# Kernel optimization log

Measured on AMD Instinct MI355X. Metric: run time of the kernel, lower is better.

## Reference

```python
import jax, jax.numpy as jnp
import numpy as np
from jax import lax

B, T, K = 2048, 1024, 8  # batch, max seq len, num_tags


def setup_inputs() -> dict:
    key = jax.random.key(0)
    k1, k2, k3, k4, k5, k6, k7 = jax.random.split(key, 7)
    score = jax.random.normal(k1, (B, T, K), jnp.float32)
    log_p = jax.nn.log_softmax(jax.random.normal(k2, (B, T, K), jnp.float32), axis=-1)
    tags = jax.random.randint(k3, (B, T), 0, K)
    seq_l = jax.random.randint(k4, (B,), 1, T + 1)  # valid lengths in [1, T]
    transitions = jax.random.normal(k5, (K, K), jnp.float32) * 0.1
    start_transitions = jax.random.normal(k6, (K,), jnp.float32) * 0.1
    end_transitions = jax.random.normal(k7, (K,), jnp.float32) * 0.1
    return {
        "log_p": log_p,
        "score": score,
        "transitions": transitions,
        "start_transitions": start_transitions,
        "end_transitions": end_transitions,
        "tags": tags,
        "seq_l": seq_l,
    }


def _crf_nll(score, tags, mask, transitions, start_transitions, end_transitions):
    """Linear-chain CRF negative log-likelihood, summed over the batch.
    score: [B,T,K] emissions; tags: [B,T] gold; mask: [B,T] bool."""
    maskf = mask.astype(score.dtype)

    # ---- numerator: score of the gold tag path ----
    emit = jnp.take_along_axis(score, tags[..., None], axis=-1)[..., 0]  # [B,T]
    num = (emit * maskf).sum(-1)
    num = num + start_transitions[tags[:, 0]]
    trans_sc = transitions[tags[:, :-1], tags[:, 1:]]  # [B,T-1]
    num = num + (trans_sc * maskf[:, 1:]).sum(-1)
    last_idx = (mask.sum(-1).astype(jnp.int32) - 1)  # [B]
    last_tag = jnp.take_along_axis(tags, last_idx[:, None], axis=1)[:, 0]
    num = num + end_transitions[last_tag]

    # ---- denominator: log partition via log-sum-exp scan over time ----
    alpha0 = start_transitions[None, :] + score[:, 0]  # [B,K]

    def step(alpha, xs):
        emit_t, mask_t = xs  # [B,K], [B]
        # alpha[b,i] + transitions[i,j] + emit[b,j], logsumexp over i
        nxt = jax.nn.logsumexp(alpha[:, :, None] + transitions[None, :, :], axis=1) + emit_t
        alpha = jnp.where(mask_t[:, None], nxt, alpha)  # freeze past end-of-seq
        return alpha, None

    xs = (jnp.swapaxes(score[:, 1:], 0, 1), jnp.swapaxes(mask[:, 1:], 0, 1))
    alpha, _ = lax.scan(step, alpha0, xs)
    log_z = jax.nn.logsumexp(alpha + end_transitions[None, :], axis=-1)  # [B]

    return -(num - log_z).sum()


def reference(log_p, score, transitions, start_transitions, end_transitions, tags, seq_l):
    mask = jnp.arange(T)[None, :] < seq_l[:, None]  # [B,T] bool
    loss = _crf_nll(score, tags, mask, transitions, start_transitions, end_transitions) / B
    # training path: quick predictions = argmax over per-token log_p, zero-padded
    pred_idx = jnp.argmax(log_p, axis=-1) * mask.astype(jnp.int64)
    return loss, pred_idx
```

## Files before the change

### kernel.cpp

```cpp
#include <hip/hip_runtime.h>
#include <hip/hip_bf16.h>


namespace {

constexpr int B = 2048;
constexpr int T = 1024;
constexpr int K = 8;
constexpr int CL = 64;
constexpr int NC = T / CL;

__device__ __forceinline__ float max8(const float* a) {
  return fmaxf(fmaxf(fmaxf(a[0], a[1]), fmaxf(a[2], a[3])),
               fmaxf(fmaxf(a[4], a[5]), fmaxf(a[6], a[7])));
}

__global__ __launch_bounds__(256) void pred_num_kernel(
    const float* __restrict__ log_p, const float* __restrict__ score,
    const float* __restrict__ trans, const float* __restrict__ start_tr,
    const float* __restrict__ end_tr, const int* __restrict__ tags,
    const int* __restrict__ seq_l, float* __restrict__ out_pred,
    float* __restrict__ ws_num) {
  int g = blockIdx.x * blockDim.x + threadIdx.x;
  int b = g >> 10;
  int t = g & (T - 1);

  const float4* lp = reinterpret_cast<const float4*>(log_p) + (g << 1);
  float4 u0 = lp[0], u1 = lp[1];
  float v[8] = {u0.x, u0.y, u0.z, u0.w, u1.x, u1.y, u1.z, u1.w};
  int best = 0;
  float bv = v[0];
#pragma unroll
  for (int j = 1; j < 8; ++j) {
    if (v[j] > bv) { bv = v[j]; best = j; }
  }

  int L = seq_l[b];
  bool act = (t < L);
  out_pred[g] = act ? (float)best : 0.0f;

  float contrib = 0.0f;
  if (act) {
    int tg = tags[g];
    contrib = score[g * 8 + tg];
    if (t == 0)
      contrib += start_tr[tg];
    else
      contrib += trans[tags[g - 1] * 8 + tg];
    if (t == L - 1) contrib += end_tr[tg];
  }
#pragma unroll
  for (int off = 32; off >= 1; off >>= 1) contrib += __shfl_down(contrib, off);
  if ((threadIdx.x & 63) == 0) atomicAdd(&ws_num[b], contrib);
}

__global__ __launch_bounds__(256) void chunk_kernel(
    const float* __restrict__ score, const float* __restrict__ trans,
    const int* __restrict__ seq_l, float* __restrict__ wsA,
    float* __restrict__ wsS) {
  int g = blockIdx.x * blockDim.x + threadIdx.x;
  int k = g & 7;
  int c = (g >> 3) & (NC - 1);
  int b = g >> 7;

  float E[8][8];
#pragma unroll
  for (int i = 0; i < 8; ++i)
#pragma unroll
    for (int j = 0; j < 8; ++j) E[i][j] = __expf(trans[i * 8 + j]);

  float a[8];
#pragma unroll
  for (int j = 0; j < 8; ++j) a[j] = (j == k) ? 1.0f : 0.0f;
  float sig = 0.0f;

  int L = seq_l[b];
  int t0 = c * CL;
  int ts = (c == 0) ? 1 : t0;
  int te = min(t0 + CL, L);
  int n = te - ts;
  const float* sp = score + ((size_t)b * T + ts) * 8;

  for (int it = 0; it < n; ++it) {
    float4 sA = *reinterpret_cast<const float4*>(sp);
    float4 sB = *reinterpret_cast<const float4*>(sp + 4);
    sp += 8;
    float em[8] = {__expf(sA.x), __expf(sA.y), __expf(sA.z), __expf(sA.w),
                   __expf(sB.x), __expf(sB.y), __expf(sB.z), __expf(sB.w)};
    float na[8];
#pragma unroll
    for (int j = 0; j < 8; ++j) {
      float acc = E[0][j] * a[0];
#pragma unroll
      for (int i = 1; i < 8; ++i) acc = fmaf(E[i][j], a[i], acc);
      na[j] = em[j] * acc;
    }
#pragma unroll
    for (int j = 0; j < 8; ++j) a[j] = na[j];
    if ((it & 7) == 7) {
      float mm = max8(a);
      float r = __builtin_amdgcn_rcpf(mm);
#pragma unroll
      for (int j = 0; j < 8; ++j) a[j] *= r;
      sig += __logf(mm);
    }
  }
  {
    float mm = max8(a);
    if (mm > 0.0f) {
      float r = __builtin_amdgcn_rcpf(mm);
#pragma unroll
      for (int j = 0; j < 8; ++j) a[j] *= r;
      sig += __logf(mm);
    }
  }

  float* Ao = wsA + (size_t)(((b * NC + c) * 8 + k) * 8);
  *reinterpret_cast<float4*>(Ao) = make_float4(a[0], a[1], a[2], a[3]);
  *reinterpret_cast<float4*>(Ao + 4) = make_float4(a[4], a[5], a[6], a[7]);
  wsS[(b * NC + c) * 8 + k] = sig;
}

__global__ __launch_bounds__(256) void combine_kernel(
    const float* __restrict__ score, const float* __restrict__ start_tr,
    const float* __restrict__ end_tr, const float* __restrict__ wsA,
    const float* __restrict__ wsS, const float* __restrict__ ws_num,
    float* __restrict__ out_loss) {
  int b = blockIdx.x * blockDim.x + threadIdx.x;

  const float* s0 = score + (size_t)b * T * 8;
  float p[8];
#pragma unroll
  for (int j = 0; j < 8; ++j) p[j] = __expf(start_tr[j] + s0[j]);
  float tau = 0.0f;
  {
    float mm = max8(p);
    float r = __builtin_amdgcn_rcpf(mm);
#pragma unroll
    for (int j = 0; j < 8; ++j) p[j] *= r;
    tau += __logf(mm);
  }

  float een[8];
#pragma unroll
  for (int j = 0; j < 8; ++j) een[j] = __expf(end_tr[j]);

  for (int c = 0; c < NC; ++c) {
    const float* Ab = wsA + (size_t)((b * NC + c) * 64);
    const float* Sb = wsS + (b * NC + c) * 8;
    float sg[8];
#pragma unroll
    for (int j = 0; j < 8; ++j) sg[j] = Sb[j];
    float smax = max8(sg);
    float w[8];
#pragma unroll
    for (int j = 0; j < 8; ++j) w[j] = p[j] * __expf(sg[j] - smax);

    float Am[8][8];
#pragma unroll
    for (int i = 0; i < 8; ++i) {
      float4 q0 = *reinterpret_cast<const float4*>(Ab + i * 8);
      float4 q1 = *reinterpret_cast<const float4*>(Ab + i * 8 + 4);
      Am[i][0] = q0.x; Am[i][1] = q0.y; Am[i][2] = q0.z; Am[i][3] = q0.w;
      Am[i][4] = q1.x; Am[i][5] = q1.y; Am[i][6] = q1.z; Am[i][7] = q1.w;
    }
    float np[8];
#pragma unroll
    for (int j = 0; j < 8; ++j) {
      float acc = Am[0][j] * w[0];
#pragma unroll
      for (int i = 1; i < 8; ++i) acc = fmaf(Am[i][j], w[i], acc);
      np[j] = acc;
    }
    tau += smax;
    float mm = max8(np);
    float r = __builtin_amdgcn_rcpf(mm);
#pragma unroll
    for (int j = 0; j < 8; ++j) p[j] = np[j] * r;
    tau += __logf(mm);
  }

  float acc = 0.0f;
#pragma unroll
  for (int j = 0; j < 8; ++j) acc = fmaf(p[j], een[j], acc);
  float logz = tau + __logf(acc);

  float part = (logz - ws_num[b]) * (1.0f / (float)B);
#pragma unroll
  for (int off = 32; off >= 1; off >>= 1) part += __shfl_down(part, off);
  if ((threadIdx.x & 63) == 0) atomicAdd(out_loss, part);
}

}

extern "C" void kernel_launch(void* const* d_in, const int* in_sizes, int n_in,
                              void* d_out, int out_size, void* d_ws,
                              size_t ws_size, hipStream_t stream) {
  const float* log_p = (const float*)d_in[0];
  const float* score = (const float*)d_in[1];
  const float* trans = (const float*)d_in[2];
  const float* start_tr = (const float*)d_in[3];
  const float* end_tr = (const float*)d_in[4];
  const int* tags = (const int*)d_in[5];
  const int* seq_l = (const int*)d_in[6];
  float* out = (float*)d_out;

  float* wsA = (float*)d_ws;
  float* wsS = wsA + (size_t)B * NC * 64;
  float* wsNum = wsS + (size_t)B * NC * 8;

  hipMemsetAsync(wsNum, 0, B * sizeof(float), stream);
  hipMemsetAsync(out, 0, sizeof(float), stream);

  pred_num_kernel<<<(B * T) / 256, 256, 0, stream>>>(
      log_p, score, trans, start_tr, end_tr, tags, seq_l, out + 1, wsNum);
  chunk_kernel<<<(B * NC * 8) / 256, 256, 0, stream>>>(score, trans, seq_l,
                                                       wsA, wsS);
  combine_kernel<<<B / 256, 256, 0, stream>>>(score, start_tr, end_tr, wsA,
                                              wsS, wsNum, out);
}
```

Before: 245.8 us.

## Parallelize CRF combine across tags and use 32 chunks when workspace allows

```diff
diff --git a/kernel.cpp b/kernel.cpp
--- a/kernel.cpp
+++ b/kernel.cpp
@@ -6,9 +6,6 @@
 
 constexpr int B = 2048;
 constexpr int T = 1024;
-constexpr int K = 8;
-constexpr int CL = 64;
-constexpr int NC = T / CL;
 
 __device__ __forceinline__ float max8(const float* a) {
   return fmaxf(fmaxf(fmaxf(a[0], a[1]), fmaxf(a[2], a[3])),
@@ -54,14 +51,16 @@
   if ((threadIdx.x & 63) == 0) atomicAdd(&ws_num[b], contrib);
 }
 
+template <int NC>
 __global__ __launch_bounds__(256) void chunk_kernel(
     const float* __restrict__ score, const float* __restrict__ trans,
     const int* __restrict__ seq_l, float* __restrict__ wsA,
     float* __restrict__ wsS) {
+  constexpr int CL = T / NC;
   int g = blockIdx.x * blockDim.x + threadIdx.x;
   int k = g & 7;
   int c = (g >> 3) & (NC - 1);
-  int b = g >> 7;
+  int b = g >> 3 >>  (NC == 32 ? 5 : 4);
 
   float E[8][8];
 #pragma unroll
@@ -115,77 +114,64 @@
     }
   }
 
-  float* Ao = wsA + (size_t)(((b * NC + c) * 8 + k) * 8);
-  *reinterpret_cast<float4*>(Ao) = make_float4(a[0], a[1], a[2], a[3]);
-  *reinterpret_cast<float4*>(Ao + 4) = make_float4(a[4], a[5], a[6], a[7]);
+  float* Ao = wsA + (size_t)(b * NC + c) * 64;
+#pragma unroll
+  for (int j = 0; j < 8; ++j) Ao[j * 8 + k] = a[j];
   wsS[(b * NC + c) * 8 + k] = sig;
 }
 
+template <int NC>
 __global__ __launch_bounds__(256) void combine_kernel(
     const float* __restrict__ score, const float* __restrict__ start_tr,
     const float* __restrict__ end_tr, const float* __restrict__ wsA,
     const float* __restrict__ wsS, const float* __restrict__ ws_num,
     float* __restrict__ out_loss) {
-  int b = blockIdx.x * blockDim.x + threadIdx.x;
-
-  const float* s0 = score + (size_t)b * T * 8;
-  float p[8];
-#pragma unroll
-  for (int j = 0; j < 8; ++j) p[j] = __expf(start_tr[j] + s0[j]);
-  float tau = 0.0f;
-  {
-    float mm = max8(p);
-    float r = __builtin_amdgcn_rcpf(mm);
-#pragma unroll
-    for (int j = 0; j < 8; ++j) p[j] *= r;
-    tau += __logf(mm);
-  }
-
-  float een[8];
-#pragma unroll
-  for (int j = 0; j < 8; ++j) een[j] = __expf(end_tr[j]);
+  int tid = blockIdx.x * blockDim.x + threadIdx.x;
+  int j = tid & 7;
+  int b = tid >> 3;
+
+  float pj = __expf(start_tr[j] + score[(size_t)b * T * 8 + j]);
+  float mm = pj;
+#pragma unroll
+  for (int m = 1; m < 8; m <<= 1) mm = fmaxf(mm, __shfl_xor(mm, m, 8));
+  float tau = __logf(mm);
+  pj *= __builtin_amdgcn_rcpf(mm);
+
+  float eej = __expf(end_tr[j]);
 
   for (int c = 0; c < NC; ++c) {
-    const float* Ab = wsA + (size_t)((b * NC + c) * 64);
-    const float* Sb = wsS + (b * NC + c) * 8;
-    float sg[8];
-#pragma unroll
-    for (int j = 0; j < 8; ++j) sg[j] = Sb[j];
-    float smax = max8(sg);
+    const float* Ab = wsA + (size_t)(b * NC + c) * 64;
+    float sgj = wsS[(b * NC + c) * 8 + j];
+    float smax = sgj;
+#pragma unroll
+    for (int m = 1; m < 8; m <<= 1) smax = fmaxf(smax, __shfl_xor(smax, m, 8));
+    float wj = pj * __expf(sgj - smax);
     float w[8];
 #pragma unroll
-    for (int j = 0; j < 8; ++j) w[j] = p[j] * __expf(sg[j] - smax);
-
-    float Am[8][8];
-#pragma unroll
-    for (int i = 0; i < 8; ++i) {
-      float4 q0 = *reinterpret_cast<const float4*>(Ab + i * 8);
-      float4 q1 = *reinterpret_cast<const float4*>(Ab + i * 8 + 4);
-      Am[i][0] = q0.x; Am[i][1] = q0.y; Am[i][2] = q0.z; Am[i][3] = q0.w;
-      Am[i][4] = q1.x; Am[i][5] = q1.y; Am[i][6] = q1.z; Am[i][7] = q1.w;
-    }
-    float np[8];
-#pragma unroll
-    for (int j = 0; j < 8; ++j) {
-      float acc = Am[0][j] * w[0];
-#pragma unroll
-      for (int i = 1; i < 8; ++i) acc = fmaf(Am[i][j], w[i], acc);
-      np[j] = acc;
-    }
-    tau += smax;
-    float mm = max8(np);
-    float r = __builtin_amdgcn_rcpf(mm);
-#pragma unroll
-    for (int j = 0; j < 8; ++j) p[j] = np[j] * r;
-    tau += __logf(mm);
-  }
-
-  float acc = 0.0f;
-#pragma unroll
-  for (int j = 0; j < 8; ++j) acc = fmaf(p[j], een[j], acc);
-  float logz = tau + __logf(acc);
-
-  float part = (logz - ws_num[b]) * (1.0f / (float)B);
+    for (int i = 0; i < 8; ++i) w[i] = __shfl(wj, i, 8);
+    float4 r0 = *reinterpret_cast<const float4*>(Ab + j * 8);
+    float4 r1 = *reinterpret_cast<const float4*>(Ab + j * 8 + 4);
+    float acc = r0.x * w[0];
+    acc = fmaf(r0.y, w[1], acc);
+    acc = fmaf(r0.z, w[2], acc);
+    acc = fmaf(r0.w, w[3], acc);
+    acc = fmaf(r1.x, w[4], acc);
+    acc = fmaf(r1.y, w[5], acc);
+    acc = fmaf(r1.z, w[6], acc);
+    acc = fmaf(r1.w, w[7], acc);
+    float mm2 = acc;
+#pragma unroll
+    for (int m = 1; m < 8; m <<= 1) mm2 = fmaxf(mm2, __shfl_xor(mm2, m, 8));
+    tau += smax + __logf(mm2);
+    pj = acc * __builtin_amdgcn_rcpf(mm2);
+  }
+
+  float term = pj * eej;
+#pragma unroll
+  for (int m = 1; m < 8; m <<= 1) term += __shfl_xor(term, m, 8);
+  float logz = tau + __logf(term);
+
+  float part = (j == 0) ? (logz - ws_num[b]) * (1.0f / (float)B) : 0.0f;
 #pragma unroll
   for (int off = 32; off >= 1; off >>= 1) part += __shfl_down(part, off);
   if ((threadIdx.x & 63) == 0) atomicAdd(out_loss, part);
@@ -205,17 +191,28 @@
   const int* seq_l = (const int*)d_in[6];
   float* out = (float*)d_out;
 
+  size_t need32 = ((size_t)B * 32 * 72 + B) * sizeof(float);
+  bool use32 = ws_size >= need32;
+  int nc = use32 ? 32 : 16;
+
   float* wsA = (float*)d_ws;
-  float* wsS = wsA + (size_t)B * NC * 64;
-  float* wsNum = wsS + (size_t)B * NC * 8;
+  float* wsS = wsA + (size_t)B * nc * 64;
+  float* wsNum = wsS + (size_t)B * nc * 8;
 
   hipMemsetAsync(wsNum, 0, B * sizeof(float), stream);
   hipMemsetAsync(out, 0, sizeof(float), stream);
 
   pred_num_kernel<<<(B * T) / 256, 256, 0, stream>>>(
       log_p, score, trans, start_tr, end_tr, tags, seq_l, out + 1, wsNum);
-  chunk_kernel<<<(B * NC * 8) / 256, 256, 0, stream>>>(score, trans, seq_l,
-                                                       wsA, wsS);
-  combine_kernel<<<B / 256, 256, 0, stream>>>(score, start_tr, end_tr, wsA,
-                                              wsS, wsNum, out);
-}
+  if (use32) {
+    chunk_kernel<32><<<(B * 32 * 8) / 256, 256, 0, stream>>>(score, trans,
+                                                             seq_l, wsA, wsS);
+    combine_kernel<32><<<(B * 8) / 256, 256, 0, stream>>>(
+        score, start_tr, end_tr, wsA, wsS, wsNum, out);
+  } else {
+    chunk_kernel<16><<<(B * 16 * 8) / 256, 256, 0, stream>>>(score, trans,
+                                                             seq_l, wsA, wsS);
+    combine_kernel<16><<<(B * 8) / 256, 256, 0, stream>>>(
+        score, start_tr, end_tr, wsA, wsS, wsNum, out);
+  }
+}
```

Measured after the change: 220.8 us. -10.1%, faster.
